# Performance work log

Hardware: AMD Instinct MI355X
Metric: run time of the kernel (lower is better)

The kernel has to match this reference:

```python
import jax, jax.numpy as jnp
import numpy as np

EPS = 1e-12
B, CNT = 4096, 2048

def setup_inputs() -> dict:
    key = jax.random.key(0)
    k1, k2, k3 = jax.random.split(key, 3)
    timestampns_set = jax.random.uniform(k1, (B, CNT), dtype=jnp.float32)
    gyro_set = jax.random.normal(k2, (B, CNT, 3), dtype=jnp.float32)
    start_quat = jax.random.normal(k3, (B, 4), dtype=jnp.float32)
    # conv1/conv2 reduce to 3x3 linear maps on the xyz axis; initialized to identity, bias 0
    W1 = jnp.eye(3, dtype=jnp.float32)
    b1 = jnp.zeros((3,), dtype=jnp.float32)
    a1 = jnp.float32(0.25)  # PReLU default, single shared parameter
    W2 = jnp.eye(3, dtype=jnp.float32)
    b2 = jnp.zeros((3,), dtype=jnp.float32)
    a2 = jnp.float32(0.25)
    return {"timestampns_set": timestampns_set, "gyro_set": gyro_set,
            "start_quat": start_quat, "W1": W1, "b1": b1, "a1": a1,
            "W2": W2, "b2": b2, "a2": a2}

def _prelu(x, a):
    return jnp.where(x >= 0, x, a * x)

def _qmul(a, b):
    aw, ax, ay, az = a[:, 0], a[:, 1], a[:, 2], a[:, 3]
    bw, bx, by, bz = b[:, 0], b[:, 1], b[:, 2], b[:, 3]
    ow = aw * bw - ax * bx - ay * by - az * bz
    ox = aw * bx + ax * bw + ay * bz - az * by
    oy = aw * by - ax * bz + ay * bw + az * bx
    oz = aw * bz + ax * by - ay * bx + az * bw
    return jnp.stack((ow, ox, oy, oz), axis=-1)

def reference(timestampns_set, gyro_set, start_quat, W1, b1, a1, W2, b2, a2):
    # calibrate_gyro: two identity-init 3x3 'convs' + PReLU, residual add
    h = _prelu(jnp.einsum('btc,oc->bto', gyro_set, W1) + b1, a1)
    g = _prelu(jnp.einsum('btc,oc->bto', h, W2) + b2, a2) + gyro_set  # [B,CNT,3]
    dt = timestampns_set[:, 1:] - timestampns_set[:, :-1]             # [B,CNT-1]
    gm = 0.5 * (g[:, :-1, :] + g[:, 1:, :])                            # midpoint gyro
    dtheta_half = gm * dt[:, :, None] * 0.5                           # [B,CNT-1,3]

    def step(q, d):
        dq = jnp.concatenate([jnp.ones((d.shape[0], 1), d.dtype), d], axis=1)
        q = _qmul(q, dq)
        n = jnp.sqrt(jnp.sum(q * q, axis=1, keepdims=True))
        q = q / jnp.maximum(n, EPS)  # F.normalize semantics
        return q, None

    q, _ = jax.lax.scan(step, start_quat, jnp.swapaxes(dtheta_half, 0, 1))
    return q
```

## Files before the change

kernel.cpp:

```cpp
#include <hip/hip_runtime.h>

#define CNT    2048
#define TPB    256
#define RPB    4
#define NCHUNK 8
#define CSTEP  256
#define GFL    768
#define BUFF   1028

struct Q { float w, x, y, z; };

__device__ __forceinline__ Q qmul(const Q a, const Q b) {
    Q o;
    o.w = fmaf(a.w, b.w, fmaf(-a.x, b.x, fmaf(-a.y, b.y, -a.z * b.z)));
    o.x = fmaf(a.w, b.x, fmaf( a.x, b.w, fmaf( a.y, b.z, -a.z * b.y)));
    o.y = fmaf(a.w, b.y, fmaf(-a.x, b.z, fmaf( a.y, b.w,  a.z * b.x)));
    o.z = fmaf(a.w, b.z, fmaf( a.x, b.y, fmaf(-a.y, b.x,  a.z * b.w)));
    return o;
}

__device__ __forceinline__ Q qmul1(const Q a, const float bx, const float by, const float bz) {
    Q o;
    o.w = fmaf(-a.x, bx, fmaf(-a.y, by, fmaf(-a.z, bz, a.w)));
    o.x = fmaf( a.w, bx, fmaf( a.y, bz, fmaf(-a.z, by, a.x)));
    o.y = fmaf( a.w, by, fmaf(-a.x, bz, fmaf( a.z, bx, a.y)));
    o.z = fmaf( a.w, bz, fmaf( a.x, by, fmaf(-a.y, bx, a.z)));
    return o;
}

__device__ __forceinline__ float prelu(const float x, const float a, const float one_m_a) {
    return fmaf(one_m_a, fmaxf(x, 0.0f), a * x);
}

__device__ __forceinline__ void dma16(const float* g, float* l) {
    __builtin_amdgcn_global_load_lds(
        (const __attribute__((address_space(1))) void*)g,
        (__attribute__((address_space(3))) void*)l,
        16, 0, 0);
}

#define WAITV(n) do { asm volatile("s_waitcnt vmcnt(" #n ")" ::: "memory"); \
                      __builtin_amdgcn_sched_barrier(0); } while (0)

__global__ __launch_bounds__(TPB) void quat_scan_kernel(
    const float* __restrict__ ts,
    const float* __restrict__ gyro,
    const float* __restrict__ sq,
    const float* __restrict__ W1, const float* __restrict__ b1, const float* __restrict__ a1p,
    const float* __restrict__ W2, const float* __restrict__ b2, const float* __restrict__ a2p,
    float* __restrict__ out,
    const int B)
{
    __shared__ float lds[RPB][2][BUFF];

    const int lane = threadIdx.x & 63;
    const int wid  = threadIdx.x >> 6;
    const int row  = blockIdx.x * RPB + wid;
    if (row >= B) return;

    float w1[9], w2[9], bb1[3], bb2[3];
    #pragma unroll
    for (int i = 0; i < 9; ++i) { w1[i] = W1[i]; w2[i] = W2[i]; }
    #pragma unroll
    for (int i = 0; i < 3; ++i) { bb1[i] = b1[i]; bb2[i] = b2[i]; }
    const float a1 = a1p[0], a2 = a2p[0];
    const float oma1 = 1.0f - a1, oma2 = 1.0f - a2;

    auto gfv = [&](const float vx, const float vy, const float vz,
                   float& gx, float& gy, float& gz) {
        float h0 = fmaf(w1[0], vx, fmaf(w1[1], vy, fmaf(w1[2], vz, bb1[0])));
        float h1 = fmaf(w1[3], vx, fmaf(w1[4], vy, fmaf(w1[5], vz, bb1[1])));
        float h2 = fmaf(w1[6], vx, fmaf(w1[7], vy, fmaf(w1[8], vz, bb1[2])));
        h0 = prelu(h0, a1, oma1);
        h1 = prelu(h1, a1, oma1);
        h2 = prelu(h2, a1, oma1);
        float u0 = fmaf(w2[0], h0, fmaf(w2[1], h1, fmaf(w2[2], h2, bb2[0])));
        float u1 = fmaf(w2[3], h0, fmaf(w2[4], h1, fmaf(w2[5], h2, bb2[1])));
        float u2 = fmaf(w2[6], h0, fmaf(w2[7], h1, fmaf(w2[8], h2, bb2[2])));
        gx = prelu(u0, a2, oma2) + vx;
        gy = prelu(u1, a2, oma2) + vy;
        gz = prelu(u2, a2, oma2) + vz;
    };

    const float* grow = gyro + (size_t)row * (CNT * 3);
    const float* trow = ts   + (size_t)row * CNT;
    float* buf0 = &lds[wid][0][0];
    float* buf1 = &lds[wid][1][0];

    auto issue = [&](const int c, float* bp) {
        const float* gs = grow + c * GFL + lane * 4;
        dma16(gs +   0, bp +   0);
        dma16(gs + 256, bp + 256);
        dma16(gs + 512, bp + 512);
        dma16(trow + c * CSTEP + lane * 4, bp + GFL);
    };

    issue(0, buf0);
    issue(1, buf1);

    Q acc = {1.0f, 0.0f, 0.0f, 0.0f};

    WAITV(4);

    for (int c = 0; c < NCHUNK; ++c) {
        float* cur = (c & 1) ? buf1 : buf0;
        float* oth = (c & 1) ? buf0 : buf1;

        const float4* gb = (const float4*)cur;
        const float4* tb = (const float4*)(cur + GFL);
        const float4 Wa = gb[3 * lane + 0];
        const float4 Wb = gb[3 * lane + 1];
        const float4 Wc = gb[3 * lane + 2];
        const float4 Wd = gb[3 * lane + 3];
        const float4 Ta = tb[lane];
        const float4 Tb = tb[lane + 1];

        Q q = {1.0f, 0.0f, 0.0f, 0.0f};
        float ax, ay, az, bx, by, bz;
        gfv(Wa.x, Wa.y, Wa.z, ax, ay, az);
        gfv(Wa.w, Wb.x, Wb.y, bx, by, bz);
        { const float s = 0.25f * (Ta.y - Ta.x);
          q = qmul1(q, (ax + bx) * s, (ay + by) * s, (az + bz) * s); }
        ax = bx; ay = by; az = bz;
        gfv(Wb.z, Wb.w, Wc.x, bx, by, bz);
        { const float s = 0.25f * (Ta.z - Ta.y);
          q = qmul1(q, (ax + bx) * s, (ay + by) * s, (az + bz) * s); }
        ax = bx; ay = by; az = bz;
        gfv(Wc.y, Wc.z, Wc.w, bx, by, bz);
        { const float s = 0.25f * (Ta.w - Ta.z);
          q = qmul1(q, (ax + bx) * s, (ay + by) * s, (az + bz) * s); }
        ax = bx; ay = by; az = bz;

        WAITV(0);
        float rx = Wd.x, ry = Wd.y, rz = Wd.z, t4 = Tb.x;
        if (c < NCHUNK - 1) {
            const float4 Xg = ((const float4*)oth)[0];
            const float  Xt = oth[GFL];
            if (lane == 63) { rx = Xg.x; ry = Xg.y; rz = Xg.z; t4 = Xt; }
        } else {
            if (lane == 63) t4 = Ta.w;
        }
        gfv(rx, ry, rz, bx, by, bz);
        { const float s = 0.25f * (t4 - Ta.w);
          q = qmul1(q, (ax + bx) * s, (ay + by) * s, (az + bz) * s); }

        {
            const float n2  = fmaf(q.w, q.w, fmaf(q.x, q.x, fmaf(q.y, q.y, q.z * q.z)));
            const float inv = 1.0f / sqrtf(n2);
            q.w *= inv; q.x *= inv; q.y *= inv; q.z *= inv;
        }

        #pragma unroll
        for (int sft = 1; sft < 64; sft <<= 1) {
            Q o;
            o.w = __shfl_down(q.w, sft);
            o.x = __shfl_down(q.x, sft);
            o.y = __shfl_down(q.y, sft);
            o.z = __shfl_down(q.z, sft);
            q = qmul(q, o);
        }
        acc = qmul(acc, q);

        if (c < NCHUNK - 2) issue(c + 2, cur);
    }

    if (lane == 0) {
        const float4 s0 = ((const float4*)(sq + (size_t)row * 4))[0];
        const Q q0 = {s0.x, s0.y, s0.z, s0.w};
        Q qf = qmul(q0, acc);
        const float n   = sqrtf(fmaf(qf.w, qf.w, fmaf(qf.x, qf.x, fmaf(qf.y, qf.y, qf.z * qf.z))));
        const float inv = 1.0f / fmaxf(n, 1e-12f);
        float4 o;
        o.x = qf.w * inv; o.y = qf.x * inv; o.z = qf.y * inv; o.w = qf.z * inv;
        ((float4*)(out + (size_t)row * 4))[0] = o;
    }
}

extern "C" void kernel_launch(void* const* d_in, const int* in_sizes, int n_in,
                              void* d_out, int out_size, void* d_ws, size_t ws_size,
                              hipStream_t stream) {
    const float* ts   = (const float*)d_in[0];
    const float* gyro = (const float*)d_in[1];
    const float* sq   = (const float*)d_in[2];
    const float* W1   = (const float*)d_in[3];
    const float* b1   = (const float*)d_in[4];
    const float* a1   = (const float*)d_in[5];
    const float* W2   = (const float*)d_in[6];
    const float* b2   = (const float*)d_in[7];
    const float* a2   = (const float*)d_in[8];
    float* out = (float*)d_out;

    const int B = in_sizes[0] / CNT;
    const int grid = (B + RPB - 1) / RPB;

    quat_scan_kernel<<<grid, TPB, 0, stream>>>(ts, gyro, sq, W1, b1, a1, W2, b2, a2, out, B);
}
```

Before: 192.6 us.

## Triple-buffer LDS DMA pipeline and fully unroll chunk loop

Moves from double to triple buffering of the per-wave LDS staging, so three chunks are in flight and each wait only needs the next chunk instead of draining all loads. The chunk loop is fully unrolled through a macro with per-iteration vmcnt thresholds, and launch bounds now request occupancy 3. This is meant to hide global-load latency better in a memory-bound kernel, at the cost of more LDS per block, which may limit occupancy, and a larger code footprint.

```diff
diff --git a/kernel.cpp b/kernel.cpp
--- a/kernel.cpp
+++ b/kernel.cpp
@@ -6,7 +6,8 @@
 #define NCHUNK 8
 #define CSTEP  256
 #define GFL    768
-#define BUFF   1028
+#define BUFF   1024
+#define WBUF   (3*BUFF+12)
 
 struct Q { float w, x, y, z; };
 
@@ -42,7 +43,7 @@
 #define WAITV(n) do { asm volatile("s_waitcnt vmcnt(" #n ")" ::: "memory"); \
                       __builtin_amdgcn_sched_barrier(0); } while (0)
 
-__global__ __launch_bounds__(TPB) void quat_scan_kernel(
+__global__ __launch_bounds__(TPB, 3) void quat_scan_kernel(
     const float* __restrict__ ts,
     const float* __restrict__ gyro,
     const float* __restrict__ sq,
@@ -51,7 +52,7 @@
     float* __restrict__ out,
     const int B)
 {
-    __shared__ float lds[RPB][2][BUFF];
+    __shared__ float lds[RPB][WBUF];
 
     const int lane = threadIdx.x & 63;
     const int wid  = threadIdx.x >> 6;
@@ -84,85 +85,85 @@
 
     const float* grow = gyro + (size_t)row * (CNT * 3);
     const float* trow = ts   + (size_t)row * CNT;
-    float* buf0 = &lds[wid][0][0];
-    float* buf1 = &lds[wid][1][0];
+    float* bufs = &lds[wid][0];
 
-    auto issue = [&](const int c, float* bp) {
+    auto issue = [&](const int c, const int k) {
         const float* gs = grow + c * GFL + lane * 4;
+        float* bp = bufs + k * BUFF;
         dma16(gs +   0, bp +   0);
         dma16(gs + 256, bp + 256);
         dma16(gs + 512, bp + 512);
         dma16(trow + c * CSTEP + lane * 4, bp + GFL);
     };
 
-    issue(0, buf0);
-    issue(1, buf1);
+    issue(0, 0); issue(1, 1); issue(2, 2);
+    Q acc = {1.0f, 0.0f, 0.0f, 0.0f};
+    WAITV(8);
 
-    Q acc = {1.0f, 0.0f, 0.0f, 0.0f};
+#define ITER(c, WVACT, PREF)                                                  \
+{                                                                             \
+    const float4* gb = (const float4*)(bufs + ((c) % 3) * BUFF);              \
+    const float4* tb = (const float4*)(bufs + ((c) % 3) * BUFF + GFL);        \
+    const float4 Wa = gb[3 * lane + 0];                                       \
+    const float4 Wb = gb[3 * lane + 1];                                       \
+    const float4 Wc_ = gb[3 * lane + 2];                                      \
+    const float4 Wd = gb[3 * lane + 3];                                       \
+    const float4 Ta = tb[lane];                                               \
+    const float4 Tb = tb[lane + 1];                                           \
+    Q q = {1.0f, 0.0f, 0.0f, 0.0f};                                           \
+    float ax, ay, az, bx, by, bz;                                             \
+    gfv(Wa.x, Wa.y, Wa.z, ax, ay, az);                                        \
+    gfv(Wa.w, Wb.x, Wb.y, bx, by, bz);                                        \
+    { const float s = 0.25f * (Ta.y - Ta.x);                                  \
+      q = qmul1(q, (ax + bx) * s, (ay + by) * s, (az + bz) * s); }            \
+    ax = bx; ay = by; az = bz;                                                \
+    gfv(Wb.z, Wb.w, Wc_.x, bx, by, bz);                                       \
+    { const float s = 0.25f * (Ta.z - Ta.y);                                  \
+      q = qmul1(q, (ax + bx) * s, (ay + by) * s, (az + bz) * s); }            \
+    ax = bx; ay = by; az = bz;                                                \
+    gfv(Wc_.y, Wc_.z, Wc_.w, bx, by, bz);                                     \
+    { const float s = 0.25f * (Ta.w - Ta.z);                                  \
+      q = qmul1(q, (ax + bx) * s, (ay + by) * s, (az + bz) * s); }            \
+    ax = bx; ay = by; az = bz;                                                \
+    WVACT;                                                                    \
+    float rx = Wd.x, ry = Wd.y, rz = Wd.z, t4 = Tb.x;                         \
+    if ((c) < NCHUNK - 1) {                                                   \
+        const float* nb = bufs + (((c) + 1) % 3) * BUFF;                      \
+        const float4 Xg = ((const float4*)nb)[0];   \
+        const float  Xt = nb[GFL];                                            \
+        if (lane == 63) { rx = Xg.x; ry = Xg.y; rz = Xg.z; t4 = Xt; }         \
+    } else {                                                                  \
+        if (lane == 63) t4 = Ta.w;          \
+    }                                                                         \
+    gfv(rx, ry, rz, bx, by, bz);                                              \
+    { const float s = 0.25f * (t4 - Ta.w);                                    \
+      q = qmul1(q, (ax + bx) * s, (ay + by) * s, (az + bz) * s); }            \
+    { const float n2  = fmaf(q.w, q.w, fmaf(q.x, q.x, fmaf(q.y, q.y, q.z * q.z))); \
+      const float inv = 1.0f / sqrtf(n2);                                     \
+      q.w *= inv; q.x *= inv; q.y *= inv; q.z *= inv; }                       \
+    _Pragma("unroll")                                                         \
+    for (int sft = 1; sft < 64; sft <<= 1) {                                  \
+        Q o;                                                                  \
+        o.w = __shfl_down(q.w, sft);                                          \
+        o.x = __shfl_down(q.x, sft);                                          \
+        o.y = __shfl_down(q.y, sft);                                          \
+        o.z = __shfl_down(q.z, sft);                                          \
+        q = qmul(q, o);                                                       \
+    }                                                                         \
+    acc = qmul(acc, q);                                                       \
+    PREF;                                                                     \
+}
 
-    WAITV(4);
+    ITER(0, WAITV(4), issue(3, 0))
+    ITER(1, WAITV(4), issue(4, 1))
+    ITER(2, WAITV(4), issue(5, 2))
+    ITER(3, WAITV(4), issue(6, 0))
+    ITER(4, WAITV(4), issue(7, 1))
+    ITER(5, WAITV(4), )
+    ITER(6, WAITV(0), )
+    ITER(7,         , )
 
-    for (int c = 0; c < NCHUNK; ++c) {
-        float* cur = (c & 1) ? buf1 : buf0;
-        float* oth = (c & 1) ? buf0 : buf1;
-
-        const float4* gb = (const float4*)cur;
-        const float4* tb = (const float4*)(cur + GFL);
-        const float4 Wa = gb[3 * lane + 0];
-        const float4 Wb = gb[3 * lane + 1];
-        const float4 Wc = gb[3 * lane + 2];
-        const float4 Wd = gb[3 * lane + 3];
-        const float4 Ta = tb[lane];
-        const float4 Tb = tb[lane + 1];
-
-        Q q = {1.0f, 0.0f, 0.0f, 0.0f};
-        float ax, ay, az, bx, by, bz;
-        gfv(Wa.x, Wa.y, Wa.z, ax, ay, az);
-        gfv(Wa.w, Wb.x, Wb.y, bx, by, bz);
-        { const float s = 0.25f * (Ta.y - Ta.x);
-          q = qmul1(q, (ax + bx) * s, (ay + by) * s, (az + bz) * s); }
-        ax = bx; ay = by; az = bz;
-        gfv(Wb.z, Wb.w, Wc.x, bx, by, bz);
-        { const float s = 0.25f * (Ta.z - Ta.y);
-          q = qmul1(q, (ax + bx) * s, (ay + by) * s, (az + bz) * s); }
-        ax = bx; ay = by; az = bz;
-        gfv(Wc.y, Wc.z, Wc.w, bx, by, bz);
-        { const float s = 0.25f * (Ta.w - Ta.z);
-          q = qmul1(q, (ax + bx) * s, (ay + by) * s, (az + bz) * s); }
-        ax = bx; ay = by; az = bz;
-
-        WAITV(0);
-        float rx = Wd.x, ry = Wd.y, rz = Wd.z, t4 = Tb.x;
-        if (c < NCHUNK - 1) {
-            const float4 Xg = ((const float4*)oth)[0];
-            const float  Xt = oth[GFL];
-            if (lane == 63) { rx = Xg.x; ry = Xg.y; rz = Xg.z; t4 = Xt; }
-        } else {
-            if (lane == 63) t4 = Ta.w;
-        }
-        gfv(rx, ry, rz, bx, by, bz);
-        { const float s = 0.25f * (t4 - Ta.w);
-          q = qmul1(q, (ax + bx) * s, (ay + by) * s, (az + bz) * s); }
-
-        {
-            const float n2  = fmaf(q.w, q.w, fmaf(q.x, q.x, fmaf(q.y, q.y, q.z * q.z)));
-            const float inv = 1.0f / sqrtf(n2);
-            q.w *= inv; q.x *= inv; q.y *= inv; q.z *= inv;
-        }
-
-        #pragma unroll
-        for (int sft = 1; sft < 64; sft <<= 1) {
-            Q o;
-            o.w = __shfl_down(q.w, sft);
-            o.x = __shfl_down(q.x, sft);
-            o.y = __shfl_down(q.y, sft);
-            o.z = __shfl_down(q.z, sft);
-            q = qmul(q, o);
-        }
-        acc = qmul(acc, q);
-
-        if (c < NCHUNK - 2) issue(c + 2, cur);
-    }
+#undef ITER
 
     if (lane == 0) {
         const float4 s0 = ((const float4*)(sq + (size_t)row * 4))[0];
```

New measurement: 195.1 us. About the same (+1.3%).
